# Kernel optimization log

Hardware: AMD Instinct MI355X
Metric: run time of the kernel (lower is better)

The kernel has to match this reference:

```python
import jax, jax.numpy as jnp
import numpy as np

N, D, C = 16384, 1024, 1024
EPS = 1e-6       # F.pairwise_distance eps added to the difference
DENOM_EPS = 1e-5


def setup_inputs() -> dict:
    key = jax.random.key(0)
    k1, k2, k3 = jax.random.split(key, 3)
    features = jax.random.normal(k1, (N, D), dtype=jnp.float32)
    labels = jax.random.randint(k2, (N,), 0, 10, dtype=jnp.int64)
    centers = jax.random.normal(k3, (C, D), dtype=jnp.float32)
    return {"features": features, "labels": labels, "centers": centers}


def reference(features, labels, centers):
    # torch: dist = ||f - c + eps||_2 per (sample, center) pair.
    # Expand exactly: ||f - c + eps||^2 = ||f||^2 + ||c||^2 - 2 f.c
    #                 + 2*eps*(sum(f) - sum(c)) + eps^2 * D
    f2 = jnp.sum(features * features, axis=1)            # [N]
    c2 = jnp.sum(centers * centers, axis=1)              # [C]
    fc = features @ centers.T                            # [N, C]
    fs = jnp.sum(features, axis=1)                       # [N]
    cs = jnp.sum(centers, axis=1)                        # [C]
    d = features.shape[1]
    sq = (f2[:, None] + c2[None, :] - 2.0 * fc
          + 2.0 * EPS * (fs[:, None] - cs[None, :]) + (EPS * EPS) * d)
    dist = jnp.sqrt(jnp.maximum(sq, 0.0))                # [N, C]
    min_dist = jnp.min(dist, axis=1)                     # [N]
    mask = (labels == 0).astype(min_dist.dtype)          # select label==0 samples
    count = jnp.sum(mask)
    loss = jnp.sum(min_dist * mask) / (count + DENOM_EPS)
    return loss
```

## Files before the change

kernel.cpp:

```cpp
#include <hip/hip_runtime.h>


constexpr int N = 16384;
constexpr int D = 1024;
constexpr int C = 1024;
constexpr float EPS = 1e-6f;

constexpr int SB = 16;
constexpr int CB = 128;
constexpr int BK = 64;
constexpr int NSPLIT = C / CB;

typedef __attribute__((ext_vector_type(8))) short bf16x8;
typedef __attribute__((ext_vector_type(4))) float f32x4;

__device__ inline unsigned mapf(float f) {
  unsigned b = __float_as_uint(f);
  return (b & 0x80000000u) ? ~b : (b | 0x80000000u);
}
__device__ inline float unmapf(unsigned u) {
  return __uint_as_float((u & 0x80000000u) ? (u ^ 0x80000000u) : ~u);
}

__device__ inline unsigned short f2bf(float x) {
  unsigned u = __float_as_uint(x);
  return (unsigned short)((u + 0x7FFFu + ((u >> 16) & 1u)) >> 16);
}

#define GLOAD_LDS16(gp, lp)                                        \
  __builtin_amdgcn_global_load_lds(                                \
      (const __attribute__((address_space(1))) void*)(gp),         \
      (__attribute__((address_space(3))) void*)(lp), 16, 0, 0)

__global__ __launch_bounds__(256) void k_setup(const float* __restrict__ cent,
                                               const int* __restrict__ labels,
                                               unsigned* __restrict__ count,
                                               unsigned* __restrict__ sel,
                                               unsigned* __restrict__ minmapped,
                                               float* __restrict__ cc,
                                               unsigned short* __restrict__ cent_bf) {
  int b = blockIdx.x, t = threadIdx.x;
  int n = b * 256 + t;
  minmapped[n] = 0xFFFFFFFFu;
  if (labels[n] == 0) {
    unsigned slot = atomicAdd(count, 1u);
    sel[slot] = (unsigned)n;
  }
  size_t base = (size_t)b * 16 * D;
#pragma unroll
  for (int u = 0; u < 16; ++u) {
    size_t off = base + (size_t)(u * 256 + t) * 4;
    float4 v = *(const float4*)(cent + off);
    short4 s4 = make_short4((short)f2bf(v.x), (short)f2bf(v.y),
                            (short)f2bf(v.z), (short)f2bf(v.w));
    *(short4*)(cent_bf + off) = s4;
  }
  int w = t >> 6, lane = t & 63;
#pragma unroll
  for (int e = 0; e < 4; ++e) {
    int c = b * 16 + w * 4 + e;
    const float* row = cent + (size_t)c * D;
    float s1 = 0.f, s2 = 0.f;
#pragma unroll
    for (int j = 0; j < D / 64; ++j) {
      float v = row[lane + 64 * j];
      s1 += v;
      s2 += v * v;
    }
#pragma unroll
    for (int off = 32; off; off >>= 1) {
      s1 += __shfl_down(s1, off);
      s2 += __shfl_down(s2, off);
    }
    if (lane == 0) cc[c] = s2 - 2.0f * EPS * s1;
  }
}

__global__ __launch_bounds__(256) void k_dist(const float* __restrict__ feat,
                                              const unsigned short* __restrict__ cent_bf,
                                              const float* __restrict__ cc,
                                              const unsigned* __restrict__ count,
                                              const unsigned* __restrict__ sel,
                                              unsigned* __restrict__ minmapped) {
  __shared__ __align__(16) unsigned short Cb[CB * BK];
  __shared__ __align__(16) unsigned short Fb[SB * BK];
  __shared__ unsigned rows[SB];

  unsigned cnt = *count;
  unsigned sbase = blockIdx.x * SB;
  if (sbase >= cnt) return;
  unsigned cbase = blockIdx.y * CB;

  int tid = threadIdx.x;
  int lane = tid & 63, w = tid >> 6;

  if (tid < SB) rows[tid] = sel[min(sbase + (unsigned)tid, cnt - 1u)];
  __syncthreads();

  int fs = tid >> 4;
  int fk4 = (tid & 15) * 4;
  const float* fsrc = feat + (size_t)rows[fs] * D + fk4;
  int fj = fk4 >> 3, fhalf = (fk4 >> 2) & 1;
  int foff = fs * BK + ((fj ^ (fs & 7)) << 3) + (fhalf << 2);

  f32x4 acc0 = {0.f, 0.f, 0.f, 0.f}, acc1 = {0.f, 0.f, 0.f, 0.f};
  int arow = lane & 15, kg = lane >> 4;
  int c0 = w * 32 + (lane & 15), c1 = c0 + 16;

  for (int t = 0; t < D / BK; ++t) {
    int kbase = t * BK;
#pragma unroll
    for (int u = 0; u < 4; ++u) {
      int chunk = (w * 4 + u) * 64 + lane;
      int r = chunk >> 3, j = chunk & 7;
      int jsrc = j ^ (r & 7);
      const unsigned short* src =
          cent_bf + (size_t)(cbase + r) * D + kbase + jsrc * 8;
      GLOAD_LDS16(src, &Cb[chunk * 8]);
    }
    {
      float4 v = *(const float4*)(fsrc + kbase);
      *(short4*)&Fb[foff] = make_short4((short)f2bf(v.x), (short)f2bf(v.y),
                                        (short)f2bf(v.z), (short)f2bf(v.w));
    }
    __syncthreads();

#pragma unroll
    for (int ks = 0; ks < 2; ++ks) {
      int jj = (ks << 2) + kg;
      bf16x8 a = *(const bf16x8*)&Fb[arow * BK + ((jj ^ (arow & 7)) << 3)];
      bf16x8 b0 = *(const bf16x8*)&Cb[c0 * BK + ((jj ^ (c0 & 7)) << 3)];
      bf16x8 b1 = *(const bf16x8*)&Cb[c1 * BK + ((jj ^ (c1 & 7)) << 3)];
      acc0 = __builtin_amdgcn_mfma_f32_16x16x32_bf16(a, b0, acc0, 0, 0, 0);
      acc1 = __builtin_amdgcn_mfma_f32_16x16x32_bf16(a, b1, acc1, 0, 0, 0);
    }
    __syncthreads();
  }

  float ccv0 = cc[cbase + c0];
  float ccv1 = cc[cbase + c1];
#pragma unroll
  for (int reg = 0; reg < 4; ++reg) {
    float v = fminf(ccv0 - 2.0f * acc0[reg], ccv1 - 2.0f * acc1[reg]);
#pragma unroll
    for (int off = 1; off < 16; off <<= 1) v = fminf(v, __shfl_xor(v, off));
    if ((lane & 15) == 0) {
      unsigned sidx = sbase + (unsigned)((lane >> 4) * 4 + reg);
      if (sidx < cnt) atomicMin(&minmapped[sidx], mapf(v));
    }
  }
}

__global__ __launch_bounds__(256) void k_final_out(const float* __restrict__ feat,
                                                   const unsigned* __restrict__ count,
                                                   const unsigned* __restrict__ sel,
                                                   const unsigned* __restrict__ minmapped,
                                                   float* __restrict__ num,
                                                   unsigned* __restrict__ done,
                                                   float* __restrict__ out) {
  unsigned cnt = *count;
  unsigned w = blockIdx.x * 4 + (threadIdx.x >> 6);
  int lane = threadIdx.x & 63;
  unsigned stride = gridDim.x * 4;
  for (unsigned slot = w; slot < cnt; slot += stride) {
    const float* row = feat + (size_t)sel[slot] * D;
    float s1 = 0.f, s2 = 0.f;
#pragma unroll
    for (int j = 0; j < D / 64; ++j) {
      float v = row[lane + 64 * j];
      s1 += v;
      s2 += v * v;
    }
#pragma unroll
    for (int off = 32; off; off >>= 1) {
      s1 += __shfl_down(s1, off);
      s2 += __shfl_down(s2, off);
    }
    if (lane == 0) {
      float ff = s2 + 2.0f * EPS * s1 + EPS * EPS * (float)D;
      float sq = ff + unmapf(minmapped[slot]);
      atomicAdd(num, sqrtf(fmaxf(sq, 0.0f)));
    }
  }
  __syncthreads();
  if (threadIdx.x == 0) {
    __threadfence();
    unsigned v = atomicAdd(done, 1u);
    if (v == gridDim.x - 1) {
      float total = atomicAdd(num, 0.0f);
      out[0] = total / ((float)cnt + 1e-5f);
    }
  }
}

extern "C" void kernel_launch(void* const* d_in, const int* in_sizes, int n_in,
                              void* d_out, int out_size, void* d_ws, size_t ws_size,
                              hipStream_t stream) {
  const float* feat = (const float*)d_in[0];
  const int* labels = (const int*)d_in[1];
  const float* cent = (const float*)d_in[2];
  float* out = (float*)d_out;

  char* ws = (char*)d_ws;
  unsigned* count = (unsigned*)ws;
  float* num = (float*)(ws + 4);
  unsigned* done = (unsigned*)(ws + 8);
  unsigned* minmapped = (unsigned*)(ws + 16);
  unsigned* sel = (unsigned*)(ws + 16 + 4 * (size_t)N);
  float* cc = (float*)(ws + 16 + 8 * (size_t)N);
  unsigned short* cent_bf =
      (unsigned short*)(ws + 16 + 8 * (size_t)N + 4 * (size_t)C);

  hipMemsetAsync(d_ws, 0, 16, stream);
  k_setup<<<64, 256, 0, stream>>>(cent, labels, count, sel, minmapped, cc,
                                  cent_bf);

  dim3 gd(N / SB, NSPLIT);
  k_dist<<<gd, 256, 0, stream>>>(feat, cent_bf, cc, count, sel, minmapped);

  k_final_out<<<128, 256, 0, stream>>>(feat, count, sel, minmapped, num, done, out);
}
```

Before: 154.8 us.

## Fuse setup, distance and reduction into one cooperative persistent kernel

Replaces the three separate launches with one cooperative kernel of 512 persistent blocks that runs init, the bf16 MFMA distance GEMM and the final reduction as phases separated by grid-wide syncs. Distance work is handed out in a grid-stride loop over (sample block, center block) tiles rather than a 2D grid with early exit, so only tiles holding selected samples are visited. Cross-phase reads and writes go through atomics to avoid stale caches. It saves launch gaps but adds grid-sync cost, atomic-load overhead and limits concurrency to 512 blocks; a three-kernel fallback runs if the cooperative launch fails.

```diff
diff --git a/kernel.cpp b/kernel.cpp
--- a/kernel.cpp
+++ b/kernel.cpp
@@ -1,4 +1,7 @@
 #include <hip/hip_runtime.h>
+#include <hip/hip_cooperative_groups.h>
+
+namespace cg = cooperative_groups;
 
 
 constexpr int N = 16384;
@@ -9,10 +12,25 @@
 constexpr int SB = 16;
 constexpr int CB = 128;
 constexpr int BK = 64;
-constexpr int NSPLIT = C / CB;
+constexpr int TPB = 256;
+constexpr int COOP_GRID = 512;
 
 typedef __attribute__((ext_vector_type(8))) short bf16x8;
 typedef __attribute__((ext_vector_type(4))) float f32x4;
+
+struct Ctx {
+  const float* feat;
+  const int* labels;
+  const float* cent;
+  unsigned* count;
+  float* num;
+  unsigned* done;
+  unsigned* minmapped;
+  unsigned* sel;
+  float* cc;
+  unsigned short* cent_bf;
+  float* out;
+};
 
 __device__ inline unsigned mapf(float f) {
   unsigned b = __float_as_uint(f);
@@ -32,34 +50,127 @@
       (const __attribute__((address_space(1))) void*)(gp),         \
       (__attribute__((address_space(3))) void*)(lp), 16, 0, 0)
 
-__global__ __launch_bounds__(256) void k_setup(const float* __restrict__ cent,
-                                               const int* __restrict__ labels,
-                                               unsigned* __restrict__ count,
-                                               unsigned* __restrict__ sel,
-                                               unsigned* __restrict__ minmapped,
-                                               float* __restrict__ cc,
-                                               unsigned short* __restrict__ cent_bf) {
-  int b = blockIdx.x, t = threadIdx.x;
-  int n = b * 256 + t;
-  minmapped[n] = 0xFFFFFFFFu;
-  if (labels[n] == 0) {
-    unsigned slot = atomicAdd(count, 1u);
-    sel[slot] = (unsigned)n;
-  }
-  size_t base = (size_t)b * 16 * D;
-#pragma unroll
-  for (int u = 0; u < 16; ++u) {
-    size_t off = base + (size_t)(u * 256 + t) * 4;
-    float4 v = *(const float4*)(cent + off);
-    short4 s4 = make_short4((short)f2bf(v.x), (short)f2bf(v.y),
-                            (short)f2bf(v.z), (short)f2bf(v.w));
-    *(short4*)(cent_bf + off) = s4;
-  }
-  int w = t >> 6, lane = t & 63;
-#pragma unroll
-  for (int e = 0; e < 4; ++e) {
-    int c = b * 16 + w * 4 + e;
-    const float* row = cent + (size_t)c * D;
+__device__ void phase_init(const Ctx& c, float* red, int b, int gs) {
+  const int t = threadIdx.x;
+  const int lane = t & 63, w = t >> 6;
+  for (int n = b * TPB + t; n < N; n += gs * TPB) {
+    atomicExch(&c.minmapped[n], 0xFFFFFFFFu);
+    if (c.labels[n] == 0) {
+      unsigned slot = atomicAdd(c.count, 1u);
+      atomicExch(&c.sel[slot], (unsigned)n);
+    }
+  }
+  for (int r = b; r < C; r += gs) {
+    const float* row = c.cent + (size_t)r * D;
+    float4 v = *(const float4*)(row + t * 4);
+    *(short4*)(c.cent_bf + (size_t)r * D + t * 4) =
+        make_short4((short)f2bf(v.x), (short)f2bf(v.y), (short)f2bf(v.z),
+                    (short)f2bf(v.w));
+    float s1 = v.x + v.y + v.z + v.w;
+    float s2 = v.x * v.x + v.y * v.y + v.z * v.z + v.w * v.w;
+#pragma unroll
+    for (int off = 32; off; off >>= 1) {
+      s1 += __shfl_down(s1, off);
+      s2 += __shfl_down(s2, off);
+    }
+    if (lane == 0) { red[w] = s1; red[4 + w] = s2; }
+    __syncthreads();
+    if (t == 0) {
+      float a1 = red[0] + red[1] + red[2] + red[3];
+      float a2 = red[4] + red[5] + red[6] + red[7];
+      atomicExch(&c.cc[r], a2 - 2.0f * EPS * a1);
+    }
+    __syncthreads();
+  }
+}
+
+__device__ void phase_dist(const Ctx& c, unsigned short* Cb, unsigned short* Fb,
+                           unsigned* rows_s, unsigned* cnt_p, int b, int gs) {
+  const int t = threadIdx.x;
+  const int lane = t & 63, w = t >> 6;
+  if (t == 0) *cnt_p = atomicAdd(c.count, 0u);
+  __syncthreads();
+  const unsigned cnt = *cnt_p;
+  const unsigned nwork = ((cnt + SB - 1) / SB) * (C / CB);
+
+  const int fs_ = t >> 4;
+  const int fk4 = (t & 15) * 4;
+  const int fj = fk4 >> 3, fhalf = (fk4 >> 2) & 1;
+  const int foff = fs_ * BK + ((fj ^ (fs_ & 7)) << 3) + (fhalf << 2);
+  const int arow = lane & 15, kg = lane >> 4;
+  const int c0 = w * 32 + (lane & 15), c1 = c0 + 16;
+
+  for (unsigned wk = (unsigned)b; wk < nwork; wk += (unsigned)gs) {
+    const unsigned sbase = (wk >> 3) * SB;
+    const unsigned cbase = (wk & 7) * CB;
+
+    if (t < SB)
+      rows_s[t] = atomicAdd(&c.sel[min(sbase + (unsigned)t, cnt - 1u)], 0u);
+    __syncthreads();
+
+    const float* fsrc = c.feat + (size_t)rows_s[fs_] * D + fk4;
+    f32x4 acc0 = {0.f, 0.f, 0.f, 0.f}, acc1 = {0.f, 0.f, 0.f, 0.f};
+
+    for (int kt = 0; kt < D / BK; ++kt) {
+      const int kbase = kt * BK;
+#pragma unroll
+      for (int u = 0; u < 4; ++u) {
+        int chunk = (w * 4 + u) * 64 + lane;
+        int r = chunk >> 3, j = chunk & 7;
+        int jsrc = j ^ (r & 7);
+        const unsigned short* src =
+            c.cent_bf + (size_t)(cbase + r) * D + kbase + jsrc * 8;
+        GLOAD_LDS16(src, Cb + chunk * 8);
+      }
+      {
+        float4 v = *(const float4*)(fsrc + kbase);
+        *(short4*)(Fb + foff) = make_short4((short)f2bf(v.x), (short)f2bf(v.y),
+                                            (short)f2bf(v.z), (short)f2bf(v.w));
+      }
+      __syncthreads();
+
+#pragma unroll
+      for (int ks = 0; ks < 2; ++ks) {
+        int jj = (ks << 2) + kg;
+        bf16x8 a = *(const bf16x8*)(Fb + arow * BK + ((jj ^ (arow & 7)) << 3));
+        bf16x8 b0 = *(const bf16x8*)(Cb + c0 * BK + ((jj ^ (c0 & 7)) << 3));
+        bf16x8 b1 = *(const bf16x8*)(Cb + c1 * BK + ((jj ^ (c1 & 7)) << 3));
+        acc0 = __builtin_amdgcn_mfma_f32_16x16x32_bf16(a, b0, acc0, 0, 0, 0);
+        acc1 = __builtin_amdgcn_mfma_f32_16x16x32_bf16(a, b1, acc1, 0, 0, 0);
+      }
+      __syncthreads();
+    }
+
+    float ccv0 = atomicAdd(&c.cc[cbase + c0], 0.0f);
+    float ccv1 = atomicAdd(&c.cc[cbase + c1], 0.0f);
+#pragma unroll
+    for (int reg = 0; reg < 4; ++reg) {
+      float v = fminf(ccv0 - 2.0f * acc0[reg], ccv1 - 2.0f * acc1[reg]);
+#pragma unroll
+      for (int off = 1; off < 16; off <<= 1) v = fminf(v, __shfl_xor(v, off));
+      if ((lane & 15) == 0) {
+        unsigned sidx = sbase + (unsigned)((lane >> 4) * 4 + reg);
+        if (sidx < cnt) atomicMin(&c.minmapped[sidx], mapf(v));
+      }
+    }
+    __syncthreads();
+  }
+}
+
+__device__ void phase_reduce(const Ctx& c, unsigned* cnt_p, int b, int gs,
+                             unsigned nblocks) {
+  const int t = threadIdx.x;
+  const int lane = t & 63, w = t >> 6;
+  if (t == 0) *cnt_p = atomicAdd(c.count, 0u);
+  __syncthreads();
+  const unsigned cnt = *cnt_p;
+
+  for (unsigned slot = (unsigned)(b * 4 + w); slot < cnt;
+       slot += (unsigned)gs * 4) {
+    unsigned srow = 0;
+    if (lane == 0) srow = atomicAdd(&c.sel[slot], 0u);
+    srow = __shfl(srow, 0);
+    const float* row = c.feat + (size_t)srow * D;
     float s1 = 0.f, s2 = 0.f;
 #pragma unroll
     for (int j = 0; j < D / 64; ++j) {
@@ -72,151 +183,86 @@
       s1 += __shfl_down(s1, off);
       s2 += __shfl_down(s2, off);
     }
-    if (lane == 0) cc[c] = s2 - 2.0f * EPS * s1;
-  }
-}
-
-__global__ __launch_bounds__(256) void k_dist(const float* __restrict__ feat,
-                                              const unsigned short* __restrict__ cent_bf,
-                                              const float* __restrict__ cc,
-                                              const unsigned* __restrict__ count,
-                                              const unsigned* __restrict__ sel,
-                                              unsigned* __restrict__ minmapped) {
+    if (lane == 0) {
+      float ff = s2 + 2.0f * EPS * s1 + EPS * EPS * (float)D;
+      float sq = ff + unmapf(atomicAdd(&c.minmapped[slot], 0u));
+      atomicAdd(c.num, sqrtf(fmaxf(sq, 0.0f)));
+    }
+  }
+  __syncthreads();
+  if (t == 0) {
+    __threadfence();
+    unsigned v = atomicAdd(c.done, 1u);
+    if (v == nblocks - 1u) {
+      float total = atomicAdd(c.num, 0.0f);
+      c.out[0] = total / ((float)cnt + 1e-5f);
+    }
+  }
+}
+
+struct ShmAll {
+  unsigned short Cb[CB * BK];
+  unsigned short Fb[SB * BK];
+  unsigned rows[SB];
+  float red[8];
+  unsigned cnt;
+};
+
+__global__ __launch_bounds__(TPB, 2) void k_all(Ctx c) {
+  __shared__ __align__(16) ShmAll sh;
+  cg::grid_group g = cg::this_grid();
+  const int b = blockIdx.x, gs = gridDim.x;
+  phase_init(c, sh.red, b, gs);
+  __threadfence();
+  g.sync();
+  phase_dist(c, sh.Cb, sh.Fb, sh.rows, &sh.cnt, b, gs);
+  __threadfence();
+  g.sync();
+  phase_reduce(c, &sh.cnt, b, gs, (unsigned)gs);
+}
+
+__global__ __launch_bounds__(TPB) void k_init(Ctx c) {
+  __shared__ float red[8];
+  phase_init(c, red, blockIdx.x, gridDim.x);
+}
+__global__ __launch_bounds__(TPB) void k_dist2(Ctx c) {
   __shared__ __align__(16) unsigned short Cb[CB * BK];
   __shared__ __align__(16) unsigned short Fb[SB * BK];
   __shared__ unsigned rows[SB];
-
-  unsigned cnt = *count;
-  unsigned sbase = blockIdx.x * SB;
-  if (sbase >= cnt) return;
-  unsigned cbase = blockIdx.y * CB;
-
-  int tid = threadIdx.x;
-  int lane = tid & 63, w = tid >> 6;
-
-  if (tid < SB) rows[tid] = sel[min(sbase + (unsigned)tid, cnt - 1u)];
-  __syncthreads();
-
-  int fs = tid >> 4;
-  int fk4 = (tid & 15) * 4;
-  const float* fsrc = feat + (size_t)rows[fs] * D + fk4;
-  int fj = fk4 >> 3, fhalf = (fk4 >> 2) & 1;
-  int foff = fs * BK + ((fj ^ (fs & 7)) << 3) + (fhalf << 2);
-
-  f32x4 acc0 = {0.f, 0.f, 0.f, 0.f}, acc1 = {0.f, 0.f, 0.f, 0.f};
-  int arow = lane & 15, kg = lane >> 4;
-  int c0 = w * 32 + (lane & 15), c1 = c0 + 16;
-
-  for (int t = 0; t < D / BK; ++t) {
-    int kbase = t * BK;
-#pragma unroll
-    for (int u = 0; u < 4; ++u) {
-      int chunk = (w * 4 + u) * 64 + lane;
-      int r = chunk >> 3, j = chunk & 7;
-      int jsrc = j ^ (r & 7);
-      const unsigned short* src =
-          cent_bf + (size_t)(cbase + r) * D + kbase + jsrc * 8;
-      GLOAD_LDS16(src, &Cb[chunk * 8]);
-    }
-    {
-      float4 v = *(const float4*)(fsrc + kbase);
-      *(short4*)&Fb[foff] = make_short4((short)f2bf(v.x), (short)f2bf(v.y),
-                                        (short)f2bf(v.z), (short)f2bf(v.w));
-    }
-    __syncthreads();
-
-#pragma unroll
-    for (int ks = 0; ks < 2; ++ks) {
-      int jj = (ks << 2) + kg;
-      bf16x8 a = *(const bf16x8*)&Fb[arow * BK + ((jj ^ (arow & 7)) << 3)];
-      bf16x8 b0 = *(const bf16x8*)&Cb[c0 * BK + ((jj ^ (c0 & 7)) << 3)];
-      bf16x8 b1 = *(const bf16x8*)&Cb[c1 * BK + ((jj ^ (c1 & 7)) << 3)];
-      acc0 = __builtin_amdgcn_mfma_f32_16x16x32_bf16(a, b0, acc0, 0, 0, 0);
-      acc1 = __builtin_amdgcn_mfma_f32_16x16x32_bf16(a, b1, acc1, 0, 0, 0);
-    }
-    __syncthreads();
-  }
-
-  float ccv0 = cc[cbase + c0];
-  float ccv1 = cc[cbase + c1];
-#pragma unroll
-  for (int reg = 0; reg < 4; ++reg) {
-    float v = fminf(ccv0 - 2.0f * acc0[reg], ccv1 - 2.0f * acc1[reg]);
-#pragma unroll
-    for (int off = 1; off < 16; off <<= 1) v = fminf(v, __shfl_xor(v, off));
-    if ((lane & 15) == 0) {
-      unsigned sidx = sbase + (unsigned)((lane >> 4) * 4 + reg);
-      if (sidx < cnt) atomicMin(&minmapped[sidx], mapf(v));
-    }
-  }
-}
-
-__global__ __launch_bounds__(256) void k_final_out(const float* __restrict__ feat,
-                                                   const unsigned* __restrict__ count,
-                                                   const unsigned* __restrict__ sel,
-                                                   const unsigned* __restrict__ minmapped,
-                                                   float* __restrict__ num,
-                                                   unsigned* __restrict__ done,
-                                                   float* __restrict__ out) {
-  unsigned cnt = *count;
-  unsigned w = blockIdx.x * 4 + (threadIdx.x >> 6);
-  int lane = threadIdx.x & 63;
-  unsigned stride = gridDim.x * 4;
-  for (unsigned slot = w; slot < cnt; slot += stride) {
-    const float* row = feat + (size_t)sel[slot] * D;
-    float s1 = 0.f, s2 = 0.f;
-#pragma unroll
-    for (int j = 0; j < D / 64; ++j) {
-      float v = row[lane + 64 * j];
-      s1 += v;
-      s2 += v * v;
-    }
-#pragma unroll
-    for (int off = 32; off; off >>= 1) {
-      s1 += __shfl_down(s1, off);
-      s2 += __shfl_down(s2, off);
-    }
-    if (lane == 0) {
-      float ff = s2 + 2.0f * EPS * s1 + EPS * EPS * (float)D;
-      float sq = ff + unmapf(minmapped[slot]);
-      atomicAdd(num, sqrtf(fmaxf(sq, 0.0f)));
-    }
-  }
-  __syncthreads();
-  if (threadIdx.x == 0) {
-    __threadfence();
-    unsigned v = atomicAdd(done, 1u);
-    if (v == gridDim.x - 1) {
-      float total = atomicAdd(num, 0.0f);
-      out[0] = total / ((float)cnt + 1e-5f);
-    }
-  }
+  __shared__ unsigned cnt;
+  phase_dist(c, Cb, Fb, rows, &cnt, blockIdx.x, gridDim.x);
+}
+__global__ __launch_bounds__(TPB) void k_red(Ctx c) {
+  __shared__ unsigned cnt;
+  phase_reduce(c, &cnt, blockIdx.x, gridDim.x, (unsigned)gridDim.x);
 }
 
 extern "C" void kernel_launch(void* const* d_in, const int* in_sizes, int n_in,
                               void* d_out, int out_size, void* d_ws, size_t ws_size,
                               hipStream_t stream) {
-  const float* feat = (const float*)d_in[0];
-  const int* labels = (const int*)d_in[1];
-  const float* cent = (const float*)d_in[2];
-  float* out = (float*)d_out;
-
   char* ws = (char*)d_ws;
-  unsigned* count = (unsigned*)ws;
-  float* num = (float*)(ws + 4);
-  unsigned* done = (unsigned*)(ws + 8);
-  unsigned* minmapped = (unsigned*)(ws + 16);
-  unsigned* sel = (unsigned*)(ws + 16 + 4 * (size_t)N);
-  float* cc = (float*)(ws + 16 + 8 * (size_t)N);
-  unsigned short* cent_bf =
+  Ctx c;
+  c.feat = (const float*)d_in[0];
+  c.labels = (const int*)d_in[1];
+  c.cent = (const float*)d_in[2];
+  c.out = (float*)d_out;
+  c.count = (unsigned*)ws;
+  c.num = (float*)(ws + 4);
+  c.done = (unsigned*)(ws + 8);
+  c.minmapped = (unsigned*)(ws + 16);
+  c.sel = (unsigned*)(ws + 16 + 4 * (size_t)N);
+  c.cc = (float*)(ws + 16 + 8 * (size_t)N);
+  c.cent_bf =
       (unsigned short*)(ws + 16 + 8 * (size_t)N + 4 * (size_t)C);
 
   hipMemsetAsync(d_ws, 0, 16, stream);
-  k_setup<<<64, 256, 0, stream>>>(cent, labels, count, sel, minmapped, cc,
-                                  cent_bf);
-
-  dim3 gd(N / SB, NSPLIT);
-  k_dist<<<gd, 256, 0, stream>>>(feat, cent_bf, cc, count, sel, minmapped);
-
-  k_final_out<<<128, 256, 0, stream>>>(feat, count, sel, minmapped, num, done, out);
-}
+
+  void* args[] = {(void*)&c};
+  hipError_t e = hipLaunchCooperativeKernel((void*)k_all, dim3(COOP_GRID),
+                                            dim3(TPB), args, 0, stream);
+  if (e != hipSuccess) {
+    k_init<<<1024, TPB, 0, stream>>>(c);
+    k_dist2<<<1024, TPB, 0, stream>>>(c);
+    k_red<<<256, TPB, 0, stream>>>(c);
+  }
+}
```

Measured after the change: 394.6 us. 2.55x slower.

## Persistent-grid distance kernel, move feature norms into setup, simplify final reduce

Applied to the files above, without the earlier changes.

The distance kernel now runs as a fixed grid of 1024 persistent blocks that walk (sample-tile, center-tile) work items. Before, it launched a 2D grid sized for all N samples, and most of those blocks exited early. Setup now runs 1024 blocks, one center row each, and also computes the per-sample feature norms for label-0 rows. The final kernel is reduced to a plain elementwise sum with one atomic per wavefront. This removes launch overhead from empty blocks and cuts the per-slot global atomics, at the cost of serial per-row loops in setup and a persistent loop that may balance work less evenly.

```diff
diff --git a/kernel.cpp b/kernel.cpp
--- a/kernel.cpp
+++ b/kernel.cpp
@@ -9,7 +9,8 @@
 constexpr int SB = 16;
 constexpr int CB = 128;
 constexpr int BK = 64;
-constexpr int NSPLIT = C / CB;
+constexpr int TPB = 256;
+constexpr int DIST_GRID = 1024;
 
 typedef __attribute__((ext_vector_type(8))) short bf16x8;
 typedef __attribute__((ext_vector_type(4))) float f32x4;
@@ -32,161 +33,177 @@
       (const __attribute__((address_space(1))) void*)(gp),         \
       (__attribute__((address_space(3))) void*)(lp), 16, 0, 0)
 
-__global__ __launch_bounds__(256) void k_setup(const float* __restrict__ cent,
-                                               const int* __restrict__ labels,
-                                               unsigned* __restrict__ count,
-                                               unsigned* __restrict__ sel,
-                                               unsigned* __restrict__ minmapped,
-                                               float* __restrict__ cc,
-                                               unsigned short* __restrict__ cent_bf) {
-  int b = blockIdx.x, t = threadIdx.x;
-  int n = b * 256 + t;
-  minmapped[n] = 0xFFFFFFFFu;
-  if (labels[n] == 0) {
-    unsigned slot = atomicAdd(count, 1u);
-    sel[slot] = (unsigned)n;
-  }
-  size_t base = (size_t)b * 16 * D;
-#pragma unroll
-  for (int u = 0; u < 16; ++u) {
-    size_t off = base + (size_t)(u * 256 + t) * 4;
-    float4 v = *(const float4*)(cent + off);
-    short4 s4 = make_short4((short)f2bf(v.x), (short)f2bf(v.y),
-                            (short)f2bf(v.z), (short)f2bf(v.w));
-    *(short4*)(cent_bf + off) = s4;
-  }
-  int w = t >> 6, lane = t & 63;
-#pragma unroll
-  for (int e = 0; e < 4; ++e) {
-    int c = b * 16 + w * 4 + e;
-    const float* row = cent + (size_t)c * D;
-    float s1 = 0.f, s2 = 0.f;
-#pragma unroll
-    for (int j = 0; j < D / 64; ++j) {
-      float v = row[lane + 64 * j];
-      s1 += v;
-      s2 += v * v;
-    }
+__global__ __launch_bounds__(TPB) void k_setup(
+    const float* __restrict__ feat, const int* __restrict__ labels,
+    const float* __restrict__ cent, unsigned* __restrict__ count,
+    unsigned* __restrict__ sel, unsigned* __restrict__ minmapped,
+    float* __restrict__ cc, float* __restrict__ ff,
+    unsigned short* __restrict__ cent_bf) {
+  __shared__ float red[8];
+  __shared__ unsigned lrow[16], lslot[16];
+  __shared__ int lcount;
+
+  const int b = blockIdx.x, t = threadIdx.x;
+  const int lane = t & 63, w = t >> 6;
+
+  if (t == 0) lcount = 0;
+  __syncthreads();
+
+  if (t < 16) {
+    int n = b * 16 + t;
+    minmapped[n] = 0xFFFFFFFFu;
+    if (labels[n] == 0) {
+      unsigned slot = atomicAdd(count, 1u);
+      sel[slot] = (unsigned)n;
+      int li = atomicAdd(&lcount, 1);
+      lrow[li] = (unsigned)n;
+      lslot[li] = slot;
+    }
+  }
+
+  {
+    const float* row = cent + (size_t)b * D;
+    float4 v = *(const float4*)(row + t * 4);
+    *(short4*)(cent_bf + (size_t)b * D + t * 4) =
+        make_short4((short)f2bf(v.x), (short)f2bf(v.y), (short)f2bf(v.z),
+                    (short)f2bf(v.w));
+    float s1 = v.x + v.y + v.z + v.w;
+    float s2 = v.x * v.x + v.y * v.y + v.z * v.z + v.w * v.w;
 #pragma unroll
     for (int off = 32; off; off >>= 1) {
       s1 += __shfl_down(s1, off);
       s2 += __shfl_down(s2, off);
     }
-    if (lane == 0) cc[c] = s2 - 2.0f * EPS * s1;
-  }
-}
-
-__global__ __launch_bounds__(256) void k_dist(const float* __restrict__ feat,
-                                              const unsigned short* __restrict__ cent_bf,
-                                              const float* __restrict__ cc,
-                                              const unsigned* __restrict__ count,
-                                              const unsigned* __restrict__ sel,
-                                              unsigned* __restrict__ minmapped) {
-  __shared__ __align__(16) unsigned short Cb[CB * BK];
-  __shared__ __align__(16) unsigned short Fb[SB * BK];
-  __shared__ unsigned rows[SB];
-
-  unsigned cnt = *count;
-  unsigned sbase = blockIdx.x * SB;
-  if (sbase >= cnt) return;
-  unsigned cbase = blockIdx.y * CB;
-
-  int tid = threadIdx.x;
-  int lane = tid & 63, w = tid >> 6;
-
-  if (tid < SB) rows[tid] = sel[min(sbase + (unsigned)tid, cnt - 1u)];
-  __syncthreads();
-
-  int fs = tid >> 4;
-  int fk4 = (tid & 15) * 4;
-  const float* fsrc = feat + (size_t)rows[fs] * D + fk4;
-  int fj = fk4 >> 3, fhalf = (fk4 >> 2) & 1;
-  int foff = fs * BK + ((fj ^ (fs & 7)) << 3) + (fhalf << 2);
-
-  f32x4 acc0 = {0.f, 0.f, 0.f, 0.f}, acc1 = {0.f, 0.f, 0.f, 0.f};
-  int arow = lane & 15, kg = lane >> 4;
-  int c0 = w * 32 + (lane & 15), c1 = c0 + 16;
-
-  for (int t = 0; t < D / BK; ++t) {
-    int kbase = t * BK;
-#pragma unroll
-    for (int u = 0; u < 4; ++u) {
-      int chunk = (w * 4 + u) * 64 + lane;
-      int r = chunk >> 3, j = chunk & 7;
-      int jsrc = j ^ (r & 7);
-      const unsigned short* src =
-          cent_bf + (size_t)(cbase + r) * D + kbase + jsrc * 8;
-      GLOAD_LDS16(src, &Cb[chunk * 8]);
-    }
-    {
-      float4 v = *(const float4*)(fsrc + kbase);
-      *(short4*)&Fb[foff] = make_short4((short)f2bf(v.x), (short)f2bf(v.y),
-                                        (short)f2bf(v.z), (short)f2bf(v.w));
-    }
-    __syncthreads();
-
-#pragma unroll
-    for (int ks = 0; ks < 2; ++ks) {
-      int jj = (ks << 2) + kg;
-      bf16x8 a = *(const bf16x8*)&Fb[arow * BK + ((jj ^ (arow & 7)) << 3)];
-      bf16x8 b0 = *(const bf16x8*)&Cb[c0 * BK + ((jj ^ (c0 & 7)) << 3)];
-      bf16x8 b1 = *(const bf16x8*)&Cb[c1 * BK + ((jj ^ (c1 & 7)) << 3)];
-      acc0 = __builtin_amdgcn_mfma_f32_16x16x32_bf16(a, b0, acc0, 0, 0, 0);
-      acc1 = __builtin_amdgcn_mfma_f32_16x16x32_bf16(a, b1, acc1, 0, 0, 0);
-    }
-    __syncthreads();
-  }
-
-  float ccv0 = cc[cbase + c0];
-  float ccv1 = cc[cbase + c1];
-#pragma unroll
-  for (int reg = 0; reg < 4; ++reg) {
-    float v = fminf(ccv0 - 2.0f * acc0[reg], ccv1 - 2.0f * acc1[reg]);
-#pragma unroll
-    for (int off = 1; off < 16; off <<= 1) v = fminf(v, __shfl_xor(v, off));
-    if ((lane & 15) == 0) {
-      unsigned sidx = sbase + (unsigned)((lane >> 4) * 4 + reg);
-      if (sidx < cnt) atomicMin(&minmapped[sidx], mapf(v));
-    }
-  }
-}
-
-__global__ __launch_bounds__(256) void k_final_out(const float* __restrict__ feat,
-                                                   const unsigned* __restrict__ count,
-                                                   const unsigned* __restrict__ sel,
-                                                   const unsigned* __restrict__ minmapped,
-                                                   float* __restrict__ num,
-                                                   unsigned* __restrict__ done,
-                                                   float* __restrict__ out) {
-  unsigned cnt = *count;
-  unsigned w = blockIdx.x * 4 + (threadIdx.x >> 6);
-  int lane = threadIdx.x & 63;
-  unsigned stride = gridDim.x * 4;
-  for (unsigned slot = w; slot < cnt; slot += stride) {
-    const float* row = feat + (size_t)sel[slot] * D;
-    float s1 = 0.f, s2 = 0.f;
-#pragma unroll
-    for (int j = 0; j < D / 64; ++j) {
-      float v = row[lane + 64 * j];
-      s1 += v;
-      s2 += v * v;
-    }
+    if (lane == 0) { red[w] = s1; red[4 + w] = s2; }
+    __syncthreads();
+    if (t == 0) {
+      float a1 = red[0] + red[1] + red[2] + red[3];
+      float a2 = red[4] + red[5] + red[6] + red[7];
+      cc[b] = a2 - 2.0f * EPS * a1;
+    }
+  }
+
+  const int nl = lcount;
+  for (int i = 0; i < nl; ++i) {
+    __syncthreads();
+    const float* row = feat + (size_t)lrow[i] * D;
+    float4 v = *(const float4*)(row + t * 4);
+    float s1 = v.x + v.y + v.z + v.w;
+    float s2 = v.x * v.x + v.y * v.y + v.z * v.z + v.w * v.w;
 #pragma unroll
     for (int off = 32; off; off >>= 1) {
       s1 += __shfl_down(s1, off);
       s2 += __shfl_down(s2, off);
     }
-    if (lane == 0) {
-      float ff = s2 + 2.0f * EPS * s1 + EPS * EPS * (float)D;
-      float sq = ff + unmapf(minmapped[slot]);
-      atomicAdd(num, sqrtf(fmaxf(sq, 0.0f)));
-    }
-  }
+    if (lane == 0) { red[w] = s1; red[4 + w] = s2; }
+    __syncthreads();
+    if (t == 0) {
+      float a1 = red[0] + red[1] + red[2] + red[3];
+      float a2 = red[4] + red[5] + red[6] + red[7];
+      ff[lslot[i]] = a2 + 2.0f * EPS * a1 + EPS * EPS * (float)D;
+    }
+  }
+}
+
+__global__ __launch_bounds__(TPB) void k_dist(
+    const float* __restrict__ feat, const unsigned short* __restrict__ cent_bf,
+    const float* __restrict__ cc, const unsigned* __restrict__ count,
+    const unsigned* __restrict__ sel, unsigned* __restrict__ minmapped) {
+  __shared__ __align__(16) unsigned short Cb[CB * BK];
+  __shared__ __align__(16) unsigned short Fb[SB * BK];
+  __shared__ unsigned rows_s[SB];
+
+  const unsigned cnt = *count;
+  const unsigned nwork = ((cnt + SB - 1) / SB) * (C / CB);
+
+  const int t = threadIdx.x;
+  const int lane = t & 63, w = t >> 6;
+
+  const int fs_ = t >> 4;
+  const int fk4 = (t & 15) * 4;
+  const int fj = fk4 >> 3, fhalf = (fk4 >> 2) & 1;
+  const int foff = fs_ * BK + ((fj ^ (fs_ & 7)) << 3) + (fhalf << 2);
+  const int arow = lane & 15, kg = lane >> 4;
+  const int c0 = w * 32 + (lane & 15), c1 = c0 + 16;
+
+  for (unsigned wk = blockIdx.x; wk < nwork; wk += DIST_GRID) {
+    const unsigned sbase = (wk >> 3) * SB;
+    const unsigned cbase = (wk & 7) * CB;
+
+    if (t < SB) rows_s[t] = sel[min(sbase + (unsigned)t, cnt - 1u)];
+    __syncthreads();
+
+    const float* fsrc = feat + (size_t)rows_s[fs_] * D + fk4;
+    f32x4 acc0 = {0.f, 0.f, 0.f, 0.f}, acc1 = {0.f, 0.f, 0.f, 0.f};
+
+    for (int kt = 0; kt < D / BK; ++kt) {
+      const int kbase = kt * BK;
+#pragma unroll
+      for (int u = 0; u < 4; ++u) {
+        int chunk = (w * 4 + u) * 64 + lane;
+        int r = chunk >> 3, j = chunk & 7;
+        int jsrc = j ^ (r & 7);
+        const unsigned short* src =
+            cent_bf + (size_t)(cbase + r) * D + kbase + jsrc * 8;
+        GLOAD_LDS16(src, Cb + chunk * 8);
+      }
+      {
+        float4 v = *(const float4*)(fsrc + kbase);
+        *(short4*)(Fb + foff) = make_short4((short)f2bf(v.x), (short)f2bf(v.y),
+                                            (short)f2bf(v.z), (short)f2bf(v.w));
+      }
+      __syncthreads();
+
+#pragma unroll
+      for (int ks = 0; ks < 2; ++ks) {
+        int jj = (ks << 2) + kg;
+        bf16x8 a = *(const bf16x8*)(Fb + arow * BK + ((jj ^ (arow & 7)) << 3));
+        bf16x8 b0 = *(const bf16x8*)(Cb + c0 * BK + ((jj ^ (c0 & 7)) << 3));
+        bf16x8 b1 = *(const bf16x8*)(Cb + c1 * BK + ((jj ^ (c1 & 7)) << 3));
+        acc0 = __builtin_amdgcn_mfma_f32_16x16x32_bf16(a, b0, acc0, 0, 0, 0);
+        acc1 = __builtin_amdgcn_mfma_f32_16x16x32_bf16(a, b1, acc1, 0, 0, 0);
+      }
+      __syncthreads();
+    }
+
+    float ccv0 = cc[cbase + c0];
+    float ccv1 = cc[cbase + c1];
+#pragma unroll
+    for (int reg = 0; reg < 4; ++reg) {
+      float v = fminf(ccv0 - 2.0f * acc0[reg], ccv1 - 2.0f * acc1[reg]);
+#pragma unroll
+      for (int off = 1; off < 16; off <<= 1) v = fminf(v, __shfl_xor(v, off));
+      if ((lane & 15) == 0) {
+        unsigned sidx = sbase + (unsigned)((lane >> 4) * 4 + reg);
+        if (sidx < cnt) atomicMin(&minmapped[sidx], mapf(v));
+      }
+    }
+    __syncthreads();
+  }
+}
+
+__global__ __launch_bounds__(TPB) void k_final_out(
+    const unsigned* __restrict__ count, const float* __restrict__ ff,
+    const unsigned* __restrict__ minmapped, float* __restrict__ num,
+    unsigned* __restrict__ done, float* __restrict__ out) {
+  const unsigned cnt = *count;
+  const int t = threadIdx.x;
+  const int lane = t & 63;
+
+  float s = 0.f;
+  for (unsigned i = blockIdx.x * TPB + t; i < cnt; i += gridDim.x * TPB) {
+    float sq = ff[i] + unmapf(minmapped[i]);
+    s += sqrtf(fmaxf(sq, 0.0f));
+  }
+#pragma unroll
+  for (int off = 32; off; off >>= 1) s += __shfl_down(s, off);
+  if (lane == 0) atomicAdd(num, s);
+
   __syncthreads();
-  if (threadIdx.x == 0) {
+  if (t == 0) {
     __threadfence();
     unsigned v = atomicAdd(done, 1u);
-    if (v == gridDim.x - 1) {
+    if (v == gridDim.x - 1u) {
       float total = atomicAdd(num, 0.0f);
       out[0] = total / ((float)cnt + 1e-5f);
     }
@@ -208,15 +225,15 @@
   unsigned* minmapped = (unsigned*)(ws + 16);
   unsigned* sel = (unsigned*)(ws + 16 + 4 * (size_t)N);
   float* cc = (float*)(ws + 16 + 8 * (size_t)N);
+  float* ff = (float*)(ws + 16 + 8 * (size_t)N + 4 * (size_t)C);
   unsigned short* cent_bf =
-      (unsigned short*)(ws + 16 + 8 * (size_t)N + 4 * (size_t)C);
+      (unsigned short*)(ws + 16 + 12 * (size_t)N + 4 * (size_t)C);
 
   hipMemsetAsync(d_ws, 0, 16, stream);
-  k_setup<<<64, 256, 0, stream>>>(cent, labels, count, sel, minmapped, cc,
-                                  cent_bf);
-
-  dim3 gd(N / SB, NSPLIT);
-  k_dist<<<gd, 256, 0, stream>>>(feat, cent_bf, cc, count, sel, minmapped);
-
-  k_final_out<<<128, 256, 0, stream>>>(feat, count, sel, minmapped, num, done, out);
-}
+
+  k_setup<<<1024, TPB, 0, stream>>>(feat, labels, cent, count, sel, minmapped,
+                                    cc, ff, cent_bf);
+  k_dist<<<DIST_GRID, TPB, 0, stream>>>(feat, cent_bf, cc, count, sel,
+                                        minmapped);
+  k_final_out<<<32, TPB, 0, stream>>>(count, ff, minmapped, num, done, out);
+}
```

After: 140.1 us. -9.4%, faster.
